# Kernel optimization log

Measured on AMD Instinct MI355X. Metric: run time of the kernel, lower is better.

The kernel has to match this reference:

```python
import jax, jax.numpy as jnp
import numpy as np
from jax import lax


def setup_inputs() -> dict:
    key = jax.random.key(0)
    k1, k2, k3, k4 = jax.random.split(key, 4)
    B, D, L = 2, 4096, 4096
    G, HL = 256, 128
    x = jax.random.normal(k1, (B, D, L), dtype=jnp.float32)
    k = jax.random.normal(k2, (B, D, L), dtype=jnp.float32)
    q = jax.random.normal(k3, (B, D, L), dtype=jnp.float32)
    h = jax.random.normal(k4, (G, HL), dtype=jnp.float32)
    return {"x": x, "k": k, "q": q, "h": h}


def reference(x, k, q, h):
    # Hyena-SE gated causal long conv (unfused_gcg reference path, bdl layout):
    #   kx = k * x ; y = causal_depthwise_conv(kx, h) ; out = q * y
    B, D, L = x.shape
    G, HL = h.shape
    # torch ref: h.squeeze(1).repeat(d // num_groups, 1)  -> tile filters over channels
    w = jnp.tile(h, (D // G, 1))[:, None, :]  # (D, 1, HL)
    kx = k * x
    y = lax.conv_general_dilated(
        kx, w,
        window_strides=(1,),
        padding=[(HL - 1, 0)],  # causal left pad
        dimension_numbers=("NCH", "OIH", "NCH"),
        feature_group_count=D,
    )  # (B, D, L)
    return q * y
```

## Files before the change

kernel.cpp:

```cpp
#include <hip/hip_runtime.h>


#define HSE_B  2
#define HSE_D  4096
#define HSE_L  4096
#define HSE_G  256
#define HSE_HL 128

constexpr int TPB = 256;
constexpr int VPT = 16;
constexpr int PAD = 128;
constexpr int LDS_KX = PAD + HSE_L;

__device__ __forceinline__ int swiz(int i) {
    return i ^ (((i >> 5) & 7) << 2);
}

__global__ __launch_bounds__(TPB) void hyena_se_kernel(
    const float* __restrict__ x, const float* __restrict__ k,
    const float* __restrict__ q, const float* __restrict__ h,
    float* __restrict__ out)
{
    __shared__ float skx[LDS_KX];

    const int blk = blockIdx.x;
    const int d   = blk & (HSE_D - 1);
    const int g   = d & (HSE_G - 1);
    const size_t row = (size_t)blk * HSE_L;
    const int tid = threadIdx.x;
    const float* __restrict__ hrow = h + (size_t)g * HSE_HL;

    if (tid < PAD / 4) {
        ((float4*)skx)[swiz(4 * tid) >> 2] = make_float4(0.f, 0.f, 0.f, 0.f);
    }
    #pragma unroll
    for (int r = 0; r < HSE_L / (4 * TPB); ++r) {
        int pos = 4 * (tid + TPB * r);
        float4 xv = *(const float4*)(x + row + pos);
        float4 kv = *(const float4*)(k + row + pos);
        ((float4*)skx)[swiz(PAD + pos) >> 2] =
            make_float4(xv.x * kv.x, xv.y * kv.y, xv.z * kv.z, xv.w * kv.w);
    }

    const int t0 = tid * VPT;

    float4 qv[VPT / 4];
    #pragma unroll
    for (int m = 0; m < VPT / 4; ++m)
        qv[m] = *(const float4*)(q + row + t0 + 4 * m);

    __syncthreads();

    float acc[VPT];
    #pragma unroll
    for (int v = 0; v < VPT; ++v) acc[v] = 0.f;

    float w[24];
    #pragma unroll
    for (int m = 0; m < 4; ++m) {
        float4 wv = ((const float4*)skx)[swiz(t0 + 4 * m) >> 2];
        w[4*m+0] = wv.x; w[4*m+1] = wv.y; w[4*m+2] = wv.z; w[4*m+3] = wv.w;
    }

    #pragma unroll
    for (int jc = 0; jc < HSE_HL / 8; ++jc) {
        #pragma unroll
        for (int m = 0; m < 2; ++m) {
            float4 wv = ((const float4*)skx)[swiz(t0 + 8 * jc + 16 + 4 * m) >> 2];
            w[16 + 4*m + 0] = wv.x; w[16 + 4*m + 1] = wv.y;
            w[16 + 4*m + 2] = wv.z; w[16 + 4*m + 3] = wv.w;
        }
        float hf[8];
        #pragma unroll
        for (int u = 0; u < 8; ++u) hf[u] = hrow[8 * jc + u];

        #pragma unroll
        for (int v = 0; v < VPT; ++v) {
            #pragma unroll
            for (int u = 0; u < 8; ++u) {
                acc[v] = fmaf(hf[u], w[1 + v + u], acc[v]);
            }
        }
        #pragma unroll
        for (int p = 0; p < 16; ++p) w[p] = w[p + 8];
    }

    #pragma unroll
    for (int m = 0; m < VPT / 4; ++m) {
        float4 o;
        o.x = qv[m].x * acc[4*m + 0];
        o.y = qv[m].y * acc[4*m + 1];
        o.z = qv[m].z * acc[4*m + 2];
        o.w = qv[m].w * acc[4*m + 3];
        *(float4*)(out + row + t0 + 4 * m) = o;
    }
}

extern "C" void kernel_launch(void* const* d_in, const int* in_sizes, int n_in,
                              void* d_out, int out_size, void* d_ws, size_t ws_size,
                              hipStream_t stream) {
    const float* x = (const float*)d_in[0];
    const float* k = (const float*)d_in[1];
    const float* q = (const float*)d_in[2];
    const float* h = (const float*)d_in[3];
    float* o = (float*)d_out;

    dim3 grid(HSE_B * HSE_D);
    dim3 block(TPB);
    hyena_se_kernel<<<grid, block, 0, stream>>>(x, k, q, h, o);
}
```

Before: 391.2 us.

## Process four rows per block with double-buffered LDS and register prefetch

Each block now handles four consecutive channel rows instead of one and keeps two LDS buffers. While the convolution for the current row runs, the x and k values for the next row are loaded into registers and written as products into the other buffer. This is meant to hide global load latency behind the FMA work and to amortize block launch overhead. In exchange it uses twice the LDS per block, raises register pressure from the prefetched float4s under a launch-bounds hint of 4, and cuts the grid to a quarter of its former size.

```diff
diff --git a/kernel.cpp b/kernel.cpp
--- a/kernel.cpp
+++ b/kernel.cpp
@@ -7,92 +7,126 @@
 #define HSE_G  256
 #define HSE_HL 128
 
-constexpr int TPB = 256;
-constexpr int VPT = 16;
-constexpr int PAD = 128;
-constexpr int LDS_KX = PAD + HSE_L;
+constexpr int TPB  = 256;
+constexpr int VPT  = 16;
+constexpr int PAD  = 128;
+constexpr int BUFN = PAD + HSE_L;
+constexpr int ROWS = 4;
+constexpr int GRID = (HSE_B * HSE_D) / ROWS;
 
 __device__ __forceinline__ int swiz(int i) {
     return i ^ (((i >> 5) & 7) << 2);
 }
 
-__global__ __launch_bounds__(TPB) void hyena_se_kernel(
+__global__ __launch_bounds__(TPB, 4) void hyena_se_kernel(
     const float* __restrict__ x, const float* __restrict__ k,
     const float* __restrict__ q, const float* __restrict__ h,
     float* __restrict__ out)
 {
-    __shared__ float skx[LDS_KX];
+    __shared__ float skx[2 * BUFN];
 
-    const int blk = blockIdx.x;
-    const int d   = blk & (HSE_D - 1);
-    const int g   = d & (HSE_G - 1);
-    const size_t row = (size_t)blk * HSE_L;
-    const int tid = threadIdx.x;
-    const float* __restrict__ hrow = h + (size_t)g * HSE_HL;
+    const int tid  = threadIdx.x;
+    const int t0   = tid * VPT;
+    const int row0 = blockIdx.x * ROWS;
 
     if (tid < PAD / 4) {
-        ((float4*)skx)[swiz(4 * tid) >> 2] = make_float4(0.f, 0.f, 0.f, 0.f);
-    }
-    #pragma unroll
-    for (int r = 0; r < HSE_L / (4 * TPB); ++r) {
-        int pos = 4 * (tid + TPB * r);
-        float4 xv = *(const float4*)(x + row + pos);
-        float4 kv = *(const float4*)(k + row + pos);
-        ((float4*)skx)[swiz(PAD + pos) >> 2] =
-            make_float4(xv.x * kv.x, xv.y * kv.y, xv.z * kv.z, xv.w * kv.w);
+        float4 z = make_float4(0.f, 0.f, 0.f, 0.f);
+        ((float4*)skx)[swiz(4 * tid) >> 2] = z;
+        ((float4*)(skx + BUFN))[swiz(4 * tid) >> 2] = z;
     }
 
-    const int t0 = tid * VPT;
-
-    float4 qv[VPT / 4];
-    #pragma unroll
-    for (int m = 0; m < VPT / 4; ++m)
-        qv[m] = *(const float4*)(q + row + t0 + 4 * m);
-
+    {
+        const size_t row = (size_t)row0 * HSE_L;
+        #pragma unroll
+        for (int r = 0; r < HSE_L / (4 * TPB); ++r) {
+            int pos = 4 * (tid + TPB * r);
+            float4 xv = *(const float4*)(x + row + pos);
+            float4 kv = *(const float4*)(k + row + pos);
+            ((float4*)skx)[swiz(PAD + pos) >> 2] =
+                make_float4(xv.x * kv.x, xv.y * kv.y, xv.z * kv.z, xv.w * kv.w);
+        }
+    }
     __syncthreads();
 
-    float acc[VPT];
-    #pragma unroll
-    for (int v = 0; v < VPT; ++v) acc[v] = 0.f;
+    for (int rr = 0; rr < ROWS; ++rr) {
+        const int cur = rr & 1;
+        float* __restrict__ buf = skx + cur * BUFN;
+        const size_t row = (size_t)(row0 + rr) * HSE_L;
+        const int d = (row0 + rr) & (HSE_D - 1);
+        const float* __restrict__ hrow = h + (size_t)(d & (HSE_G - 1)) * HSE_HL;
 
-    float w[24];
-    #pragma unroll
-    for (int m = 0; m < 4; ++m) {
-        float4 wv = ((const float4*)skx)[swiz(t0 + 4 * m) >> 2];
-        w[4*m+0] = wv.x; w[4*m+1] = wv.y; w[4*m+2] = wv.z; w[4*m+3] = wv.w;
-    }
+        float4 qv[VPT / 4];
+        #pragma unroll
+        for (int m = 0; m < VPT / 4; ++m)
+            qv[m] = *(const float4*)(q + row + t0 + 4 * m);
 
-    #pragma unroll
-    for (int jc = 0; jc < HSE_HL / 8; ++jc) {
+        float4 xn[4], kn[4];
+        const bool more = (rr + 1 < ROWS);
+        if (more) {
+            const size_t nrow = row + HSE_L;
+            #pragma unroll
+            for (int r = 0; r < 4; ++r) {
+                int pos = 4 * (tid + TPB * r);
+                xn[r] = *(const float4*)(x + nrow + pos);
+                kn[r] = *(const float4*)(k + nrow + pos);
+            }
+        }
+
+        float acc[VPT];
         #pragma unroll
-        for (int m = 0; m < 2; ++m) {
-            float4 wv = ((const float4*)skx)[swiz(t0 + 8 * jc + 16 + 4 * m) >> 2];
-            w[16 + 4*m + 0] = wv.x; w[16 + 4*m + 1] = wv.y;
-            w[16 + 4*m + 2] = wv.z; w[16 + 4*m + 3] = wv.w;
+        for (int v = 0; v < VPT; ++v) acc[v] = 0.f;
+
+        float w[24];
+        #pragma unroll
+        for (int m = 0; m < 4; ++m) {
+            float4 wv = ((const float4*)buf)[swiz(t0 + 4 * m) >> 2];
+            w[4*m+0] = wv.x; w[4*m+1] = wv.y; w[4*m+2] = wv.z; w[4*m+3] = wv.w;
         }
-        float hf[8];
-        #pragma unroll
-        for (int u = 0; u < 8; ++u) hf[u] = hrow[8 * jc + u];
 
         #pragma unroll
-        for (int v = 0; v < VPT; ++v) {
+        for (int jc = 0; jc < HSE_HL / 8; ++jc) {
             #pragma unroll
-            for (int u = 0; u < 8; ++u) {
-                acc[v] = fmaf(hf[u], w[1 + v + u], acc[v]);
+            for (int m = 0; m < 2; ++m) {
+                float4 wv = ((const float4*)buf)[swiz(t0 + 8 * jc + 16 + 4 * m) >> 2];
+                w[16 + 4*m + 0] = wv.x; w[16 + 4*m + 1] = wv.y;
+                w[16 + 4*m + 2] = wv.z; w[16 + 4*m + 3] = wv.w;
+            }
+            float hf[8];
+            #pragma unroll
+            for (int u = 0; u < 8; ++u) hf[u] = hrow[8 * jc + u];
+
+            #pragma unroll
+            for (int v = 0; v < VPT; ++v) {
+                #pragma unroll
+                for (int u = 0; u < 8; ++u) {
+                    acc[v] = fmaf(hf[u], w[1 + v + u], acc[v]);
+                }
+            }
+            #pragma unroll
+            for (int p = 0; p < 16; ++p) w[p] = w[p + 8];
+        }
+
+        #pragma unroll
+        for (int m = 0; m < VPT / 4; ++m) {
+            float4 o;
+            o.x = qv[m].x * acc[4*m + 0];
+            o.y = qv[m].y * acc[4*m + 1];
+            o.z = qv[m].z * acc[4*m + 2];
+            o.w = qv[m].w * acc[4*m + 3];
+            *(float4*)(out + row + t0 + 4 * m) = o;
+        }
+
+        if (more) {
+            float* __restrict__ nbuf = skx + (cur ^ 1) * BUFN;
+            #pragma unroll
+            for (int r = 0; r < 4; ++r) {
+                int pos = 4 * (tid + TPB * r);
+                ((float4*)nbuf)[swiz(PAD + pos) >> 2] = make_float4(
+                    xn[r].x * kn[r].x, xn[r].y * kn[r].y,
+                    xn[r].z * kn[r].z, xn[r].w * kn[r].w);
             }
         }
-        #pragma unroll
-        for (int p = 0; p < 16; ++p) w[p] = w[p + 8];
-    }
-
-    #pragma unroll
-    for (int m = 0; m < VPT / 4; ++m) {
-        float4 o;
-        o.x = qv[m].x * acc[4*m + 0];
-        o.y = qv[m].y * acc[4*m + 1];
-        o.z = qv[m].z * acc[4*m + 2];
-        o.w = qv[m].w * acc[4*m + 3];
-        *(float4*)(out + row + t0 + 4 * m) = o;
+        __syncthreads();
     }
 }
 
@@ -105,7 +139,7 @@
     const float* h = (const float*)d_in[3];
     float* o = (float*)d_out;
 
-    dim3 grid(HSE_B * HSE_D);
+    dim3 grid(GRID);
     dim3 block(TPB);
     hyena_se_kernel<<<grid, block, 0, stream>>>(x, k, q, h, o);
 }
```

After: 460.9 us. 1.18x slower.
